# Optimization experiments

Hardware: AMD Instinct MI355X
Metric: run time of the kernel (lower is better)

## Reference

```python
import jax, jax.numpy as jnp
import numpy as np

T, B, V, E, H = 512, 64, 50000, 256, 256  # seq, batch, vocab, embed, lstm_hidden
D2 = 2 * H
NC = 5


def setup_inputs() -> dict:
    key = jax.random.key(0)
    ks = jax.random.split(key, 16)
    u = lambda k, shape, s=0.1: jax.random.uniform(k, shape, jnp.float32, -s, s)
    return {
        "embed": jax.random.randint(ks[0], (T, B), 0, V),
        "h0": jnp.zeros((2, B, H), jnp.float32),
        "c0": jnp.zeros((2, B, H), jnp.float32),
        "emb_table": jax.random.normal(ks[1], (V, E), jnp.float32),
        "Wih_f": u(ks[2], (4 * H, E)),
        "Whh_f": u(ks[3], (4 * H, H)),
        "bih_f": u(ks[4], (4 * H,)),
        "bhh_f": u(ks[5], (4 * H,)),
        "Wih_b": u(ks[6], (4 * H, E)),
        "Whh_b": u(ks[7], (4 * H, H)),
        "bih_b": u(ks[8], (4 * H,)),
        "bhh_b": u(ks[9], (4 * H,)),
        "W_word": u(ks[10], (D2, D2)),
        "b_word": u(ks[11], (D2,)),
        "proj_word": u(ks[12], (D2,)),
        "lin_W": u(ks[13], (NC, D2)),
        "lin_b": u(ks[14], (NC,)),
    }


def _lstm_dir(x, h0, c0, Wih, Whh, bih, bhh):
    # x: (T,B,E). PyTorch LSTM gate order: i, f, g, o.
    xg = jnp.einsum('tbe,ge->tbg', x, Wih) + bih + bhh  # (T,B,4H)

    def step(carry, xt):
        h, c = carry
        g = xt + h @ Whh.T
        i, f, gg, o = jnp.split(g, 4, axis=-1)
        c = jax.nn.sigmoid(f) * c + jax.nn.sigmoid(i) * jnp.tanh(gg)
        h = jax.nn.sigmoid(o) * jnp.tanh(c)
        return (h, c), h

    _, hs = jax.lax.scan(step, (h0, c0), xg)
    return hs  # (T,B,H)


def reference(embed, h0, c0, emb_table,
              Wih_f, Whh_f, bih_f, bhh_f,
              Wih_b, Whh_b, bih_b, bhh_b,
              W_word, b_word, proj_word, lin_W, lin_b):
    x = emb_table[embed]  # (T,B,E)
    out_f = _lstm_dir(x, h0[0], c0[0], Wih_f, Whh_f, bih_f, bhh_f)
    out_b = _lstm_dir(x[::-1], h0[1], c0[1], Wih_b, Whh_b, bih_b, bhh_b)[::-1]
    out = jnp.concatenate([out_f, out_b], axis=-1)  # (T,B,2H)
    # additive attention: tanh(out @ W + b) @ proj, softmax over T
    squish = jnp.tanh(jnp.einsum('tbd,de->tbe', out, W_word) + b_word)
    attn = jax.nn.softmax(jnp.einsum('tbd,d->tb', squish, proj_word), axis=0)
    vec = jnp.einsum('tb,tbd->bd', attn, out)  # (B,2H)
    return vec @ lin_W.T + lin_b  # (B, n_classes)
```

## Files before the change

kernel.cpp:

```cpp
#include <hip/hip_runtime.h>
#include <hip/hip_fp16.h>
#include <cstdint>
#include <cstddef>

#define TT 512
#define BB 64
#define EE 256
#define HH 256
#define G4 1024
#define DD 512
#define NCLS 5
#define CH 64
#define NCH (TT / CH)

typedef _Float16 half8 __attribute__((ext_vector_type(8)));
typedef float f32x4 __attribute__((ext_vector_type(4)));

#define OFF_XGF   0ull
#define OFF_XGB   8388608ull
#define OFF_OUTB  16777216ull
#define OFF_WHHF  50331648ull
#define OFF_WIHF  51380224ull
#define OFF_BIAS  52428800ull
#define OFF_HST   52436992ull
#define OFF_CST   52568064ull
#define OFF_LOG   52699136ull
#define OFF_ATT   52830208ull
#define OFF_HEX   52961280ull
#define OFF_FLG   53092352ull

__device__ __forceinline__ f32x4 mfma16(half8 a, half8 b, f32x4 c) {
  return __builtin_amdgcn_mfma_f32_16x16x32_f16(a, b, c, 0, 0, 0);
}
__device__ __forceinline__ float sigm(float x) {
  return __fdividef(1.f, 1.f + __expf(-x));
}
__device__ __forceinline__ float tanh_(float x) {
  float e = __expf(2.f * x);
  return 1.f - __fdividef(2.f, e + 1.f);
}
__device__ __forceinline__ f32x4 shflx4(f32x4 v, int mask) {
  f32x4 r;
  r[0] = __shfl_xor(v[0], mask, 64);
  r[1] = __shfl_xor(v[1], mask, 64);
  r[2] = __shfl_xor(v[2], mask, 64);
  r[3] = __shfl_xor(v[3], mask, 64);
  return r;
}

#define HSWZ(br, u) ((((br) * 256) + (u)) ^ (((br) & 7) << 3))

__global__ __launch_bounds__(256) void make_frags(
    const float* __restrict__ WhhF, const float* __restrict__ WhhB,
    const float* __restrict__ WihF, const float* __restrict__ WihB,
    __half* __restrict__ whhfrag, __half* __restrict__ wihfrag)
{
  int idx = blockIdx.x * 256 + threadIdx.x;
  int r = idx & 7, lane = (idx >> 3) & 63, ks = (idx >> 9) & 7;
  int mm = lane & 15;
  int k = ks * 32 + (lane >> 4) * 8 + r;
  if (idx < (1 << 19)) {
    int pf = (idx >> 12) & 63, d = (idx >> 18) & 1;
    const float* W = d ? WhhB : WhhF;
    int g = (mm & 3) * 256 + pf * 4 + (mm >> 2);
    whhfrag[idx] = __float2half(W[(size_t)g * HH + k]);
  } else {
    int e = idx - (1 << 19);
    int pf = (e >> 12) & 63, d = (e >> 18) & 1;
    const float* W = d ? WihB : WihF;
    int g = (mm & 3) * 256 + pf * 4 + (mm >> 2);
    wihfrag[e] = __float2half(W[(size_t)g * EE + k]);
  }
}

__global__ __launch_bounds__(256) void bias_prep(
    const float* __restrict__ bihF, const float* __restrict__ bhhF,
    const float* __restrict__ bihB, const float* __restrict__ bhhB,
    float* __restrict__ bias)
{
  int i = blockIdx.x * 256 + threadIdx.x;
  int d = i >> 10, pcol = i & 1023;
  int g = (pcol & 3) * 256 + (pcol >> 2);
  bias[i] = (d ? bihB : bihF)[g] + (d ? bhhB : bhhF)[g];
}

__global__ __launch_bounds__(256) void xg_mfma(
    int c, const int* __restrict__ embed, const float* __restrict__ emb,
    const __half* __restrict__ wihfrag, const float* __restrict__ biassum,
    __half* __restrict__ xgF, __half* __restrict__ xgB)
{
  const int d = blockIdx.z, ls = blockIdx.x, gblk = blockIdx.y;
  int t = c * CH + ls;
  if (d) t = TT - 1 - t;
  __half* xg = d ? xgB : xgF;
  const int tid = threadIdx.x, w = tid >> 6, l = tid & 63;

  __shared__ int idx[64];
  __shared__ unsigned short xs[64 * 256];

  if (tid < 64) idx[tid] = embed[t * BB + tid];
  __syncthreads();

  {
    const int rr = tid >> 2, cq = (tid & 3) * 64;
    const float* src = emb + (size_t)idx[rr] * EE + cq;
#pragma unroll
    for (int j = 0; j < 8; ++j) {
      float4 a = *(const float4*)(src + j * 8);
      float4 b = *(const float4*)(src + j * 8 + 4);
      half8 hv;
      hv[0] = (_Float16)a.x; hv[1] = (_Float16)a.y; hv[2] = (_Float16)a.z; hv[3] = (_Float16)a.w;
      hv[4] = (_Float16)b.x; hv[5] = (_Float16)b.y; hv[6] = (_Float16)b.z; hv[7] = (_Float16)b.w;
      int hidx = (rr * 256 + cq + j * 8) ^ ((rr & 7) << 3);
      *(half8*)&xs[hidx] = hv;
    }
  }
  __syncthreads();

  const __half* bfb = wihfrag + (size_t)((d * 64 + gblk * 4) * 8) * 512 + l * 8;
  half8 Bf[4][8];
#pragma unroll
  for (int ct = 0; ct < 4; ++ct)
#pragma unroll
    for (int ks = 0; ks < 8; ++ks)
      Bf[ct][ks] = *(const half8*)(bfb + (ct * 8 + ks) * 512);

  f32x4 acc[4];
#pragma unroll
  for (int ct = 0; ct < 4; ++ct) {
    float bv = biassum[d * 1024 + gblk * 64 + ct * 16 + (l & 15)];
    acc[ct][0] = bv; acc[ct][1] = bv; acc[ct][2] = bv; acc[ct][3] = bv;
  }

  const int arow = w * 16 + (l & 15);
#pragma unroll
  for (int ks = 0; ks < 8; ++ks) {
    int hidx = (arow * 256 + ks * 32 + (l >> 4) * 8) ^ ((arow & 7) << 3);
    half8 af = *(const half8*)&xs[hidx];
#pragma unroll
    for (int ct = 0; ct < 4; ++ct)
      acc[ct] = mfma16(af, Bf[ct][ks], acc[ct]);
  }

#pragma unroll
  for (int ct = 0; ct < 4; ++ct) {
    ushort4 sv;
    sv.x = __half_as_ushort(__float2half(acc[ct][0]));
    sv.y = __half_as_ushort(__float2half(acc[ct][1]));
    sv.z = __half_as_ushort(__float2half(acc[ct][2]));
    sv.w = __half_as_ushort(__float2half(acc[ct][3]));
    size_t base = ((size_t)(ls * 4 + w) * 64 + (gblk * 4 + ct)) * 256 + l * 4;
    *(ushort4*)((unsigned short*)xg + base) = sv;
  }
}

__global__ __launch_bounds__(512, 2) void scan_dist(
    int c, const __half* __restrict__ xgF, const __half* __restrict__ xgB,
    const __half* __restrict__ whhfrag,
    const float* __restrict__ hin, const float* __restrict__ cin,
    float* __restrict__ hstate, float* __restrict__ cstate,
    __half* __restrict__ outb, __half* __restrict__ hex, int* __restrict__ flags)
{
  const int d = blockIdx.y;
  const int bg = blockIdx.x >> 2, ug = blockIdx.x & 3;
  const int tid = threadIdx.x, w = tid >> 6, l = tid & 63;
  const int m = l & 15, qr = l >> 4, q = m & 3, ul = m >> 2;
  const unsigned short* xg = (const unsigned short*)(d ? xgB : xgF);

  __shared__ unsigned short hb[16 * 256];

  const int pf0 = ug * 16 + w * 2;

  half8 Wf[2][8];
#pragma unroll
  for (int cf = 0; cf < 2; ++cf)
#pragma unroll
    for (int ks = 0; ks < 8; ++ks)
      Wf[cf][ks] = *(const half8*)(whhfrag +
          ((size_t)(d * 64 + pf0 + cf) * 8 + ks) * 512 + l * 8);

#pragma unroll
  for (int i = 0; i < 8; ++i) {
    int idx = i * 512 + tid;
    int r = idx >> 8, u = idx & 255;
    hb[HSWZ(r, u)] = __half_as_ushort(
        __float2half(hin[(size_t)(d * BB + bg * 16 + r) * HH + u]));
  }
  float cst[2][4];
#pragma unroll
  for (int cf = 0; cf < 2; ++cf) {
    int U = (pf0 + cf) * 4 + ul;
#pragma unroll
    for (int j = 0; j < 4; ++j)
      cst[cf][j] = cin[(size_t)(d * BB + bg * 16 + qr * 4 + j) * HH + U];
  }
  __syncthreads();

  for (int ls = 0; ls < CH; ++ls) {
    int t = c * CH + ls;
    if (d) t = TT - 1 - t;

    ushort4 xv[2];
#pragma unroll
    for (int cf = 0; cf < 2; ++cf) {
      size_t base = ((size_t)(ls * 4 + bg) * 64 + (pf0 + cf)) * 256 + l * 4;
      xv[cf] = *(const ushort4*)(xg + base);
    }
    half8 af[8];
#pragma unroll
    for (int ks = 0; ks < 8; ++ks)
      af[ks] = *(const half8*)&hb[HSWZ(m, ks * 32 + qr * 8)];
    __syncthreads();

    f32x4 acc[2];
#pragma unroll
    for (int cf = 0; cf < 2; ++cf) {
      acc[cf][0] = __half2float(__ushort_as_half(xv[cf].x));
      acc[cf][1] = __half2float(__ushort_as_half(xv[cf].y));
      acc[cf][2] = __half2float(__ushort_as_half(xv[cf].z));
      acc[cf][3] = __half2float(__ushort_as_half(xv[cf].w));
    }
#pragma unroll
    for (int ks = 0; ks < 8; ++ks)
#pragma unroll
      for (int cf = 0; cf < 2; ++cf)
        acc[cf] = mfma16(af[ks], Wf[cf][ks], acc[cf]);

    __half* hslice = hex + (size_t)(d * 2 + (ls & 1)) * 64 * 256;
#pragma unroll
    for (int cf = 0; cf < 2; ++cf) {
      f32x4 e = acc[cf];
      f32x4 o1 = shflx4(e, 1);
      f32x4 gev = (q & 1) ? o1 : e;
      f32x4 gov = (q & 1) ? e : o1;
      f32x4 ge2 = shflx4(gev, 2);
      f32x4 go2 = shflx4(gov, 2);
      f32x4 gi = (q & 2) ? ge2 : gev;
      f32x4 gg = (q & 2) ? gev : ge2;
      f32x4 gf = (q & 2) ? go2 : gov;
      f32x4 go = (q & 2) ? gov : go2;
      int U = (pf0 + cf) * 4 + ul;
#pragma unroll
      for (int j = 0; j < 4; ++j) {
        float ig = sigm(gi[j]), fg = sigm(gf[j]);
        float gz = tanh_(gg[j]), og = sigm(go[j]);
        cst[cf][j] = fg * cst[cf][j] + ig * gz;
        float hv = og * tanh_(cst[cf][j]);
        if (q == 0) {
          int r = qr * 4 + j;
          unsigned short hu = __half_as_ushort(__float2half(hv));
          hb[HSWZ(r, U)] = hu;
          hslice[(size_t)(bg * 16 + r) * 256 + U] = __ushort_as_half(hu);
          outb[((size_t)t * BB + bg * 16 + r) * DD + d * HH + U] = __ushort_as_half(hu);
        }
      }
    }
    __syncthreads();

    const int fbase = (((d * NCH + c) * CH + ls) * 4 + bg) * 4;
    if (tid == 0)
      __hip_atomic_store(&flags[fbase + ug], 1, __ATOMIC_RELEASE,
                         __HIP_MEMORY_SCOPE_AGENT);
    if (tid < 4 && tid != ug) {
      while (__hip_atomic_load(&flags[fbase + tid], __ATOMIC_ACQUIRE,
                               __HIP_MEMORY_SCOPE_AGENT) == 0)
        __builtin_amdgcn_s_sleep(4);
    }
    __syncthreads();

    {
      const unsigned short* hsrc =
          (const unsigned short*)hex + (size_t)(d * 2 + (ls & 1)) * 64 * 256;
      int r = tid >> 5, u2 = (tid & 31) * 2;
#pragma unroll
      for (int p = 0; p < 3; ++p) {
        int peer = p + (p >= ug ? 1 : 0);
        int u = peer * 64 + u2;
        const unsigned short* s2 = hsrc + (size_t)(bg * 16 + r) * 256 + u;
        int hi = HSWZ(r, u);
        hb[hi] = s2[0];
        hb[hi + 1] = s2[1];
      }
    }
    __syncthreads();
  }

#pragma unroll
  for (int i = 0; i < 8; ++i) {
    int idx = i * 512 + tid;
    int r = idx >> 8, u = idx & 255;
    hstate[(size_t)(d * BB + bg * 16 + r) * HH + u] =
        __half2float(__ushort_as_half(hb[HSWZ(r, u)]));
  }
  if (q == 0) {
#pragma unroll
    for (int cf = 0; cf < 2; ++cf) {
      int U = (pf0 + cf) * 4 + ul;
#pragma unroll
      for (int j = 0; j < 4; ++j)
        cstate[(size_t)(d * BB + bg * 16 + qr * 4 + j) * HH + U] = cst[cf][j];
    }
  }
}

__global__ __launch_bounds__(1024, 1) void squish_logits(
    const __half* __restrict__ outb, const float* __restrict__ Ww,
    const float* __restrict__ bw, const float* __restrict__ proj,
    float* __restrict__ logits)
{
  const int r0 = blockIdx.x * 64;
  const int tid = threadIdx.x;
  const int tm = tid >> 6;
  const int tn = tid & 63;
  __shared__ float As[16][68];
  __shared__ float Bs[16][516];
  __shared__ float red[64][65];

  float acc[4][8] = {};
  const int am = tid >> 4, ak = tid & 15;
  const int bk = tid >> 7, bn = (tid & 127) * 4;

  for (int k0 = 0; k0 < DD; k0 += 16) {
    float a0 = __half2float(outb[(size_t)(r0 + am) * DD + k0 + ak]);
    float4 b0 = *(const float4*)&Ww[(size_t)(k0 + bk) * DD + bn];
    float4 b1 = *(const float4*)&Ww[(size_t)(k0 + bk + 8) * DD + bn];
    __syncthreads();
    As[ak][am] = a0;
    *(float4*)&Bs[bk][bn] = b0;
    *(float4*)&Bs[bk + 8][bn] = b1;
    __syncthreads();
#pragma unroll
    for (int k = 0; k < 16; ++k) {
      float4 a = *(const float4*)&As[k][tm * 4];
      float4 p0 = *(const float4*)&Bs[k][tn * 8];
      float4 p1 = *(const float4*)&Bs[k][tn * 8 + 4];
      float av[4] = {a.x, a.y, a.z, a.w};
#pragma unroll
      for (int i = 0; i < 4; ++i) {
        acc[i][0] += av[i] * p0.x; acc[i][1] += av[i] * p0.y;
        acc[i][2] += av[i] * p0.z; acc[i][3] += av[i] * p0.w;
        acc[i][4] += av[i] * p1.x; acc[i][5] += av[i] * p1.y;
        acc[i][6] += av[i] * p1.z; acc[i][7] += av[i] * p1.w;
      }
    }
  }
  float partial[4] = {0.f, 0.f, 0.f, 0.f};
#pragma unroll
  for (int jj = 0; jj < 8; ++jj) {
    int col = tn * 8 + jj;
    float bwv = bw[col], pv = proj[col];
#pragma unroll
    for (int i = 0; i < 4; ++i)
      partial[i] += tanhf(acc[i][jj] + bwv) * pv;
  }
#pragma unroll
  for (int i = 0; i < 4; ++i) red[tm * 4 + i][tn] = partial[i];
  __syncthreads();
  if (tid < 64) {
    float s = 0.f;
    for (int x = 0; x < 64; ++x) s += red[tid][x];
    logits[r0 + tid] = s;
  }
}

__global__ __launch_bounds__(256) void softmax_t(const float* __restrict__ logits,
                                                 float* __restrict__ attn)
{
  const int b = blockIdx.x;
  const int tid = threadIdx.x;
  __shared__ float sm[256];
  float v0 = logits[tid * BB + b];
  float v1 = logits[(tid + 256) * BB + b];
  sm[tid] = fmaxf(v0, v1);
  __syncthreads();
  for (int s = 128; s > 0; s >>= 1) {
    if (tid < s) sm[tid] = fmaxf(sm[tid], sm[tid + s]);
    __syncthreads();
  }
  float M = sm[0];
  __syncthreads();
  float e0 = expf(v0 - M), e1 = expf(v1 - M);
  sm[tid] = e0 + e1;
  __syncthreads();
  for (int s = 128; s > 0; s >>= 1) {
    if (tid < s) sm[tid] += sm[tid + s];
    __syncthreads();
  }
  float inv = 1.f / sm[0];
  attn[tid * BB + b] = e0 * inv;
  attn[(tid + 256) * BB + b] = e1 * inv;
}

__global__ __launch_bounds__(512) void vec_final(
    const __half* __restrict__ outb, const float* __restrict__ attn,
    const float* __restrict__ linW, const float* __restrict__ linb,
    float* __restrict__ y)
{
  const int b = blockIdx.x;
  const int d = threadIdx.x;
  float acc = 0.f;
  for (int t = 0; t < TT; ++t)
    acc += attn[t * BB + b] * __half2float(outb[((size_t)t * BB + b) * DD + d]);
  __shared__ float red[512];
  for (int cls = 0; cls < NCLS; ++cls) {
    red[d] = acc * linW[cls * DD + d];
    __syncthreads();
    for (int s = 256; s > 0; s >>= 1) {
      if (d < s) red[d] += red[d + s];
      __syncthreads();
    }
    if (d == 0) y[b * NCLS + cls] = red[0] + linb[cls];
    __syncthreads();
  }
}

extern "C" void kernel_launch(void* const* d_in, const int* in_sizes, int n_in,
                              void* d_out, int out_size, void* d_ws, size_t ws_size,
                              hipStream_t stream) {
  const int*   embed     = (const int*)d_in[0];
  const float* h0        = (const float*)d_in[1];
  const float* c0        = (const float*)d_in[2];
  const float* emb_table = (const float*)d_in[3];
  const float* Wih_f     = (const float*)d_in[4];
  const float* Whh_f     = (const float*)d_in[5];
  const float* bih_f     = (const float*)d_in[6];
  const float* bhh_f     = (const float*)d_in[7];
  const float* Wih_b     = (const float*)d_in[8];
  const float* Whh_b     = (const float*)d_in[9];
  const float* bih_b     = (const float*)d_in[10];
  const float* bhh_b     = (const float*)d_in[11];
  const float* W_word    = (const float*)d_in[12];
  const float* b_word    = (const float*)d_in[13];
  const float* proj_word = (const float*)d_in[14];
  const float* lin_W     = (const float*)d_in[15];
  const float* lin_b     = (const float*)d_in[16];

  char* ws = (char*)d_ws;
  __half* xgF     = (__half*)(ws + OFF_XGF);
  __half* xgB     = (__half*)(ws + OFF_XGB);
  __half* outb    = (__half*)(ws + OFF_OUTB);
  __half* whhfrag = (__half*)(ws + OFF_WHHF);
  __half* wihfrag = (__half*)(ws + OFF_WIHF);
  float*  biassum = (float*)(ws + OFF_BIAS);
  float*  hstate  = (float*)(ws + OFF_HST);
  float*  cstate  = (float*)(ws + OFF_CST);
  float*  logits  = (float*)(ws + OFF_LOG);
  float*  attn    = (float*)(ws + OFF_ATT);
  __half* hex     = (__half*)(ws + OFF_HEX);
  int*    flags   = (int*)(ws + OFF_FLG);

  hipMemsetAsync(flags, 0, 65536, stream);

  make_frags<<<4096, 256, 0, stream>>>(Whh_f, Whh_b, Wih_f, Wih_b, whhfrag, wihfrag);
  bias_prep<<<8, 256, 0, stream>>>(bih_f, bhh_f, bih_b, bhh_b, biassum);

  for (int c = 0; c < NCH; ++c) {
    xg_mfma<<<dim3(CH, 16, 2), 256, 0, stream>>>(c, embed, emb_table,
        wihfrag, biassum, xgF, xgB);
    const float* hin = (c == 0) ? h0 : hstate;
    const float* cin = (c == 0) ? c0 : cstate;
    scan_dist<<<dim3(16, 2), 512, 0, stream>>>(c, xgF, xgB, whhfrag,
        hin, cin, hstate, cstate, outb, hex, flags);
  }

  squish_logits<<<512, 1024, 0, stream>>>(outb, W_word, b_word, proj_word, logits);
  softmax_t<<<64, 256, 0, stream>>>(logits, attn);
  vec_final<<<64, 512, 0, stream>>>(outb, attn, lin_W, lin_b, (float*)d_out);
}
```

Baseline: 3.177 ms.

## Coalesce h-exchange stores and use relaxed atomics for cross-block LSTM sync

The per-step hidden-state exchange between the four cooperating blocks now happens after the LDS write. Each thread does one 32-bit store to the exchange buffer and to the output, replacing scattered 16-bit stores from only q==0 lanes. Release/acquire flag operations become relaxed atomics with an explicit vmcnt wait and compiler barriers, peer reads use relaxed atomic 32-bit loads, and the spin sleep is shortened. The aim is to cut per-timestep latency in the serial recurrence, at the cost of depending on manual waitcnt ordering for memory visibility, which may be fragile across caches.

```diff
diff --git a/kernel.cpp b/kernel.cpp
--- a/kernel.cpp
+++ b/kernel.cpp
@@ -196,6 +196,9 @@
   }
   __syncthreads();
 
+  const int pr = tid >> 5;
+  const int uL = (tid & 31) * 2;
+
   for (int ls = 0; ls < CH; ++ls) {
     int t = c * CH + ls;
     if (d) t = TT - 1 - t;
@@ -226,7 +229,6 @@
       for (int cf = 0; cf < 2; ++cf)
         acc[cf] = mfma16(af[ks], Wf[cf][ks], acc[cf]);
 
-    __half* hslice = hex + (size_t)(d * 2 + (ls & 1)) * 64 * 256;
 #pragma unroll
     for (int cf = 0; cf < 2; ++cf) {
       f32x4 e = acc[cf];
@@ -248,39 +250,44 @@
         float hv = og * tanh_(cst[cf][j]);
         if (q == 0) {
           int r = qr * 4 + j;
-          unsigned short hu = __half_as_ushort(__float2half(hv));
-          hb[HSWZ(r, U)] = hu;
-          hslice[(size_t)(bg * 16 + r) * 256 + U] = __ushort_as_half(hu);
-          outb[((size_t)t * BB + bg * 16 + r) * DD + d * HH + U] = __ushort_as_half(hu);
+          hb[HSWZ(r, U)] = __half_as_ushort(__float2half(hv));
         }
       }
     }
     __syncthreads();
 
+    unsigned int* hexu =
+        (unsigned int*)hex + (size_t)(d * 2 + (ls & 1)) * (64 * 256 / 2);
+    {
+      int u = ug * 64 + uL;
+      unsigned int v = *(const unsigned int*)&hb[HSWZ(pr, u)];
+      __hip_atomic_store(&hexu[((bg * 16 + pr) * 256 + u) >> 1], v,
+                         __ATOMIC_RELAXED, __HIP_MEMORY_SCOPE_AGENT);
+      *(unsigned int*)&outb[((size_t)t * BB + bg * 16 + pr) * DD + d * HH + u] =
+          v;
+    }
+    asm volatile("s_waitcnt vmcnt(0)" ::: "memory");
+    __syncthreads();
     const int fbase = (((d * NCH + c) * CH + ls) * 4 + bg) * 4;
     if (tid == 0)
-      __hip_atomic_store(&flags[fbase + ug], 1, __ATOMIC_RELEASE,
+      __hip_atomic_store(&flags[fbase + ug], 1, __ATOMIC_RELAXED,
                          __HIP_MEMORY_SCOPE_AGENT);
     if (tid < 4 && tid != ug) {
-      while (__hip_atomic_load(&flags[fbase + tid], __ATOMIC_ACQUIRE,
+      while (__hip_atomic_load(&flags[fbase + tid], __ATOMIC_RELAXED,
                                __HIP_MEMORY_SCOPE_AGENT) == 0)
-        __builtin_amdgcn_s_sleep(4);
-    }
-    __syncthreads();
-
-    {
-      const unsigned short* hsrc =
-          (const unsigned short*)hex + (size_t)(d * 2 + (ls & 1)) * 64 * 256;
-      int r = tid >> 5, u2 = (tid & 31) * 2;
-#pragma unroll
-      for (int p = 0; p < 3; ++p) {
-        int peer = p + (p >= ug ? 1 : 0);
-        int u = peer * 64 + u2;
-        const unsigned short* s2 = hsrc + (size_t)(bg * 16 + r) * 256 + u;
-        int hi = HSWZ(r, u);
-        hb[hi] = s2[0];
-        hb[hi + 1] = s2[1];
-      }
+        __builtin_amdgcn_s_sleep(1);
+    }
+    asm volatile("" ::: "memory");
+    __syncthreads();
+
+#pragma unroll
+    for (int p = 0; p < 3; ++p) {
+      int peer = p + (p >= ug ? 1 : 0);
+      int u = peer * 64 + uL;
+      unsigned int pv =
+          __hip_atomic_load(&hexu[((bg * 16 + pr) * 256 + u) >> 1],
+                            __ATOMIC_RELAXED, __HIP_MEMORY_SCOPE_AGENT);
+      *(unsigned int*)&hb[HSWZ(pr, u)] = pv;
     }
     __syncthreads();
   }
```

After: 3.375 ms. 1.06x slower.
